# Optimization experiments

Measured on AMD Instinct MI355X. Metric: run time of the kernel, lower is better.

Reference implementation:

```python
import jax, jax.numpy as jnp
import numpy as np

SH_C0 = 0.28209479177387814
SH_C1 = 0.4886025119029199
EPS2D = 0.3  # gsplat 'classic' rasterize_mode adds 0.3 to 2D covariance diagonal
NEAR_PLANE = 0.01
FAR_PLANE = 1e10
ALPHA_MIN = 1.0 / 255.0
ALPHA_MAX = 0.999
T_EPS = 1e-4  # gsplat terminates compositing when transmittance drops below this

N_GAUSS = 2048
WIDTH = 160
HEIGHT = 160


def _quat_to_rotmat(q):
    q = q / jnp.linalg.norm(q, axis=-1, keepdims=True)
    w, x, y, z = q[:, 0], q[:, 1], q[:, 2], q[:, 3]
    return jnp.stack([
        1 - 2 * (y * y + z * z), 2 * (x * y - w * z), 2 * (x * z + w * y),
        2 * (x * y + w * z), 1 - 2 * (x * x + z * z), 2 * (y * z - w * x),
        2 * (x * z - w * y), 2 * (y * z + w * x), 1 - 2 * (x * x + y * y),
    ], axis=-1).reshape(-1, 3, 3)


def _forward(means3d, opacities, scales, quats, sh0, shN, camtoworlds, Ks, width, height):
    viewmat = jnp.linalg.inv(camtoworlds)[0]  # world->cam, single camera
    K = Ks[0]
    fx, fy, cx, cy = K[0, 0], K[1, 1], K[0, 2], K[1, 2]
    opac = jax.nn.sigmoid(opacities)
    sh = jnp.concatenate([sh0, shN], axis=1)  # [N,4,3]

    # degree-1 SH -> view-dependent RGB
    campos = camtoworlds[0, :3, 3]
    d = means3d - campos
    d = d / jnp.linalg.norm(d, axis=-1, keepdims=True)
    dxv, dyv, dzv = d[:, 0:1], d[:, 1:2], d[:, 2:3]
    colors = SH_C0 * sh[:, 0] + SH_C1 * (-dyv * sh[:, 1] + dzv * sh[:, 2] - dxv * sh[:, 3]) + 0.5
    colors = jnp.maximum(colors, 0.0)  # [N,3]

    # 3D covariance = R S S^T R^T
    R = _quat_to_rotmat(quats)
    M = R * scales[:, None, :]
    cov3d = M @ jnp.swapaxes(M, 1, 2)  # [N,3,3]

    # project to camera
    W3, t3 = viewmat[:3, :3], viewmat[:3, 3]
    tcam = means3d @ W3.T + t3  # [N,3]
    tz = tcam[:, 2]
    rz = 1.0 / tz
    lim_x = 1.3 * (0.5 * width / fx)
    lim_y = 1.3 * (0.5 * height / fy)
    txz = jnp.clip(tcam[:, 0] * rz, -lim_x, lim_x)
    tyz = jnp.clip(tcam[:, 1] * rz, -lim_y, lim_y)
    zero = jnp.zeros_like(rz)
    J = jnp.stack([
        jnp.stack([fx * rz, zero, -fx * txz * rz], axis=-1),
        jnp.stack([zero, fy * rz, -fy * tyz * rz], axis=-1),
    ], axis=-2)  # [N,2,3]
    cov_cam = jnp.einsum('ij,njk,lk->nil', W3, cov3d, W3)
    cov2d = jnp.einsum('nij,njk,nlk->nil', J, cov_cam, J)  # [N,2,2]
    a = cov2d[:, 0, 0] + EPS2D
    bb = cov2d[:, 0, 1]
    c = cov2d[:, 1, 1] + EPS2D
    det = a * c - bb * bb
    det_safe = jnp.where(det > 0, det, 1.0)
    cA, cB, cC = c / det_safe, -bb / det_safe, a / det_safe  # conic
    mx = fx * tcam[:, 0] * rz + cx
    my = fy * tcam[:, 1] * rz + cy
    valid = (tz > NEAR_PLANE) & (tz < FAR_PLANE) & (det > 0)

    # global front-to-back depth sort (single camera)
    order = jnp.argsort(tz)
    mx, my = mx[order], my[order]
    cA, cB, cC = cA[order], cB[order], cC[order]
    opac_s, colors_s = opac[order], colors[order]
    tz_s, valid_s = tz[order], valid[order]

    # pixel centers, flattened row-major [P = H*W]
    xs = jnp.arange(width, dtype=means3d.dtype) + 0.5
    ys = jnp.arange(height, dtype=means3d.dtype) + 0.5
    px = jnp.tile(xs, height)
    py = jnp.repeat(ys, width)

    dx = px[:, None] - mx[None, :]  # [P,N]
    dy = py[:, None] - my[None, :]
    sigma = 0.5 * (cA[None, :] * dx * dx + cC[None, :] * dy * dy) + cB[None, :] * dx * dy
    alpha = jnp.minimum(ALPHA_MAX, opac_s[None, :] * jnp.exp(-sigma))
    keep = valid_s[None, :] & (sigma >= 0) & (alpha >= ALPHA_MIN)
    alpha = jnp.where(keep, alpha, 0.0)

    T = jnp.cumprod(1.0 - alpha, axis=-1)
    T_excl = jnp.concatenate([jnp.ones_like(T[:, :1]), T[:, :-1]], axis=-1)
    w = jnp.where(T_excl > T_EPS, alpha * T_excl, 0.0)  # [P,N]

    rgb = w @ colors_s                     # [P,3]
    depth = w @ tz_s                       # [P] accumulated depth
    alpha_tot = jnp.sum(w, axis=-1)        # [P]
    ed = depth / jnp.maximum(alpha_tot, 1e-10)  # expected depth ('ED')
    render_colors = jnp.concatenate([rgb, ed[:, None]], axis=-1).reshape(1, height, width, 4)
    render_alphas = alpha_tot.reshape(1, height, width, 1)
    return render_colors, render_alphas


def setup_inputs() -> dict:
    key = jax.random.key(0)
    ks = jax.random.split(key, 6)
    means3d = jax.random.normal(ks[0], (N_GAUSS, 3), jnp.float32) * 1.0 + jnp.array([0.0, 0.0, 4.0])
    opacities = jax.random.normal(ks[1], (N_GAUSS,), jnp.float32)
    scales = jax.random.uniform(ks[2], (N_GAUSS, 3), jnp.float32) * 0.05 + 0.01
    quats = jax.random.normal(ks[3], (N_GAUSS, 4), jnp.float32)
    sh0 = jax.random.normal(ks[4], (N_GAUSS, 1, 3), jnp.float32) * 0.5
    shN = jax.random.normal(ks[5], (N_GAUSS, 3, 3), jnp.float32) * 0.1
    camtoworlds = jnp.eye(4, dtype=jnp.float32)[None]  # camera at origin looking +z
    Ks = jnp.array([[[200.0, 0.0, WIDTH / 2.0], [0.0, 200.0, HEIGHT / 2.0], [0.0, 0.0, 1.0]]], jnp.float32)
    return {"means3d": means3d, "opacities": opacities, "scales": scales, "quats": quats,
            "sh0": sh0, "shN": shN, "camtoworlds": camtoworlds, "Ks": Ks,
            "width": WIDTH, "height": HEIGHT}


def reference(means3d, opacities, scales, quats, sh0, shN, camtoworlds, Ks, width, height):
    return _forward(means3d, opacities, scales, quats, sh0, shN, camtoworlds, Ks, width, height)
```

## Files before the change

kernel.cpp:

```cpp
#include <hip/hip_runtime.h>
#include <math.h>

#define SH_C0f 0.28209479177387814f
#define SH_C1f 0.4886025119029199f
#define EPS2D 0.3f
#define NEAR_PLANE 0.01f
#define FAR_PLANE 1e10f
#define ALPHA_MIN (1.0f/255.0f)
#define ALPHA_MAX 0.999f
#define T_EPS 1e-4f
#define TS 8
#define NW 8

__global__ void preprocess_kernel(
    const float* __restrict__ means, const float* __restrict__ opac_in,
    const float* __restrict__ scales, const float* __restrict__ quats,
    const float* __restrict__ sh0, const float* __restrict__ shN,
    const float* __restrict__ c2w, const float* __restrict__ Ks,
    const int* __restrict__ wptr, const int* __restrict__ hptr,
    float4* __restrict__ attrs, float* __restrict__ tz_arr, int N)
{
    int i = blockIdx.x * blockDim.x + threadIdx.x;
    if (i >= N) return;

    float m[16];
    #pragma unroll
    for (int k = 0; k < 16; k++) m[k] = c2w[k];
    float inv[12];
    inv[0]  =  m[5]*m[10]*m[15] - m[5]*m[11]*m[14] - m[9]*m[6]*m[15] + m[9]*m[7]*m[14] + m[13]*m[6]*m[11] - m[13]*m[7]*m[10];
    inv[4]  = -m[4]*m[10]*m[15] + m[4]*m[11]*m[14] + m[8]*m[6]*m[15] - m[8]*m[7]*m[14] - m[12]*m[6]*m[11] + m[12]*m[7]*m[10];
    inv[8]  =  m[4]*m[9]*m[15]  - m[4]*m[11]*m[13] - m[8]*m[5]*m[15] + m[8]*m[7]*m[13] + m[12]*m[5]*m[11] - m[12]*m[7]*m[9];
    inv[1]  = -m[1]*m[10]*m[15] + m[1]*m[11]*m[14] + m[9]*m[2]*m[15] - m[9]*m[3]*m[14] - m[13]*m[2]*m[11] + m[13]*m[3]*m[10];
    inv[5]  =  m[0]*m[10]*m[15] - m[0]*m[11]*m[14] - m[8]*m[2]*m[15] + m[8]*m[3]*m[14] + m[12]*m[2]*m[11] - m[12]*m[3]*m[10];
    inv[9]  = -m[0]*m[9]*m[15]  + m[0]*m[11]*m[13] + m[8]*m[1]*m[15] - m[8]*m[3]*m[13] - m[12]*m[1]*m[11] + m[12]*m[3]*m[9];
    inv[2]  =  m[1]*m[6]*m[15]  - m[1]*m[7]*m[14]  - m[5]*m[2]*m[15] + m[5]*m[3]*m[14] + m[13]*m[2]*m[7]  - m[13]*m[3]*m[6];
    inv[6]  = -m[0]*m[6]*m[15]  + m[0]*m[7]*m[14]  + m[4]*m[2]*m[15] - m[4]*m[3]*m[14] - m[12]*m[2]*m[7]  + m[12]*m[3]*m[6];
    inv[10] =  m[0]*m[5]*m[15]  - m[0]*m[7]*m[13]  - m[4]*m[1]*m[15] + m[4]*m[3]*m[13] + m[12]*m[1]*m[7]  - m[12]*m[3]*m[5];
    inv[3]  = -m[1]*m[6]*m[11]  + m[1]*m[7]*m[10]  + m[5]*m[2]*m[11] - m[5]*m[3]*m[10] - m[9]*m[2]*m[7]   + m[9]*m[3]*m[6];
    inv[7]  =  m[0]*m[6]*m[11]  - m[0]*m[7]*m[10]  - m[4]*m[2]*m[11] + m[4]*m[3]*m[10] + m[8]*m[2]*m[7]   - m[8]*m[3]*m[6];
    inv[11] = -m[0]*m[5]*m[11]  + m[0]*m[7]*m[9]   + m[4]*m[1]*m[11] - m[4]*m[3]*m[9]  - m[8]*m[1]*m[7]   + m[8]*m[3]*m[5];
    {
        float inv12 = -m[4]*m[9]*m[14] + m[4]*m[10]*m[13] + m[8]*m[5]*m[14] - m[8]*m[6]*m[13] - m[12]*m[5]*m[10] + m[12]*m[6]*m[9];
        float det = m[0]*inv[0] + m[1]*inv[4] + m[2]*inv[8] + m[3]*inv12;
        float r = 1.0f / det;
        #pragma unroll
        for (int k = 0; k < 12; k++) inv[k] *= r;
    }
    const float W00 = inv[0], W01 = inv[1], W02 = inv[2],  t0 = inv[3];
    const float W10 = inv[4], W11 = inv[5], W12 = inv[6],  t1 = inv[7];
    const float W20 = inv[8], W21 = inv[9], W22 = inv[10], t2 = inv[11];

    const float fx = Ks[0], cx = Ks[2], fy = Ks[4], cy = Ks[5];
    const float width = (float)wptr[0], height = (float)hptr[0];

    const float mxx = means[i*3+0], myy = means[i*3+1], mzz = means[i*3+2];

    const float cpx = m[3], cpy = m[7], cpz = m[11];
    float dx = mxx - cpx, dy = myy - cpy, dz = mzz - cpz;
    float dn = sqrtf(dx*dx + dy*dy + dz*dz);
    dx /= dn; dy /= dn; dz /= dn;

    float col[3];
    #pragma unroll
    for (int c = 0; c < 3; c++) {
        float v = SH_C0f * sh0[i*3+c]
                + SH_C1f * (-dy * shN[i*9 + 0*3 + c] + dz * shN[i*9 + 1*3 + c] - dx * shN[i*9 + 2*3 + c])
                + 0.5f;
        col[c] = fmaxf(v, 0.0f);
    }

    const float op = 1.0f / (1.0f + expf(-opac_in[i]));

    float qw = quats[i*4+0], qx = quats[i*4+1], qy = quats[i*4+2], qz = quats[i*4+3];
    float qn = sqrtf(qw*qw + qx*qx + qy*qy + qz*qz);
    qw /= qn; qx /= qn; qy /= qn; qz /= qn;
    const float R00 = 1.f - 2.f*(qy*qy + qz*qz), R01 = 2.f*(qx*qy - qw*qz), R02 = 2.f*(qx*qz + qw*qy);
    const float R10 = 2.f*(qx*qy + qw*qz), R11 = 1.f - 2.f*(qx*qx + qz*qz), R12 = 2.f*(qy*qz - qw*qx);
    const float R20 = 2.f*(qx*qz - qw*qy), R21 = 2.f*(qy*qz + qw*qx), R22 = 1.f - 2.f*(qx*qx + qy*qy);

    const float sx = scales[i*3+0], sy = scales[i*3+1], sz = scales[i*3+2];
    const float M00 = R00*sx, M01 = R01*sy, M02 = R02*sz;
    const float M10 = R10*sx, M11 = R11*sy, M12 = R12*sz;
    const float M20 = R20*sx, M21 = R21*sy, M22 = R22*sz;

    const float S00 = M00*M00 + M01*M01 + M02*M02;
    const float S01 = M00*M10 + M01*M11 + M02*M12;
    const float S02 = M00*M20 + M01*M21 + M02*M22;
    const float S11 = M10*M10 + M11*M11 + M12*M12;
    const float S12 = M10*M20 + M11*M21 + M12*M22;
    const float S22 = M20*M20 + M21*M21 + M22*M22;

    const float tcx = W00*mxx + W01*myy + W02*mzz + t0;
    const float tcy = W10*mxx + W11*myy + W12*mzz + t1;
    const float tcz = W20*mxx + W21*myy + W22*mzz + t2;
    const float rz = 1.0f / tcz;

    const float limx = 1.3f * (0.5f * width / fx);
    const float limy = 1.3f * (0.5f * height / fy);
    const float txz = fminf(fmaxf(tcx * rz, -limx), limx);
    const float tyz = fminf(fmaxf(tcy * rz, -limy), limy);

    const float V00 = W00*S00 + W01*S01 + W02*S02;
    const float V01 = W00*S01 + W01*S11 + W02*S12;
    const float V02 = W00*S02 + W01*S12 + W02*S22;
    const float V10 = W10*S00 + W11*S01 + W12*S02;
    const float V11 = W10*S01 + W11*S11 + W12*S12;
    const float V12 = W10*S02 + W11*S12 + W12*S22;
    const float V20 = W20*S00 + W21*S01 + W22*S02;
    const float V21 = W20*S01 + W21*S11 + W22*S12;
    const float V22 = W20*S02 + W21*S12 + W22*S22;
    const float CC00 = V00*W00 + V01*W01 + V02*W02;
    const float CC01 = V00*W10 + V01*W11 + V02*W12;
    const float CC02 = V00*W20 + V01*W21 + V02*W22;
    const float CC11 = V10*W10 + V11*W11 + V12*W12;
    const float CC12 = V10*W20 + V11*W21 + V12*W22;
    const float CC22 = V20*W20 + V21*W21 + V22*W22;

    const float j00 = fx * rz,  j02 = -fx * txz * rz;
    const float j11 = fy * rz,  j12 = -fy * tyz * rz;

    const float u0 = j00*CC00 + j02*CC02;
    const float u1 = j00*CC01 + j02*CC12;
    const float u2 = j00*CC02 + j02*CC22;
    const float v1 = j11*CC11 + j12*CC12;
    const float v2 = j11*CC12 + j12*CC22;
    const float c2d00 = u0*j00 + u2*j02;
    const float c2d01 = u1*j11 + u2*j12;
    const float c2d11 = v1*j11 + v2*j12;

    const float a  = c2d00 + EPS2D;
    const float bb = c2d01;
    const float cc = c2d11 + EPS2D;
    const float det = a*cc - bb*bb;
    const float det_safe = (det > 0.0f) ? det : 1.0f;
    const float invd = 1.0f / det_safe;

    const bool valid = (tcz > NEAR_PLANE) && (tcz < FAR_PLANE) && (det > 0.0f);

    float rad = 0.0f;
    if (valid && op >= ALPHA_MIN) {
        const float lmax = 0.5f*(a + cc) + sqrtf(fmaxf(0.f, 0.25f*(a - cc)*(a - cc) + bb*bb));
        const float sig_cut = logf(255.0f * op);
        rad = sqrtf(fmaxf(sig_cut, 0.0f) * 2.0f * lmax) * 1.001f + 0.5f;
    }

    const float mx2d = fx * tcx * rz + cx;
    const float my2d = fy * tcy * rz + cy;

    attrs[i*3+0] = make_float4(mx2d, my2d, 0.5f * cc * invd, -bb * invd);
    attrs[i*3+1] = make_float4(0.5f * a * invd, op, tcz, rad);
    attrs[i*3+2] = make_float4(col[0], col[1], col[2], 0.0f);
    tz_arr[i] = tcz;
}

__global__ __launch_bounds__(64) void sort_scatter_kernel(
    const float* __restrict__ tz, const float4* __restrict__ attrs,
    float4* __restrict__ attrs_s, float4* __restrict__ bounds_s, int N)
{
    const int i = blockIdx.x;
    const int lane = threadIdx.x;
    const float k = tz[i];

    int rank = 0;
    int j = lane * 4;
    const int Nv = N & ~3;
    for (; j + 3 < Nv; j += 256) {
        const float4 v = *reinterpret_cast<const float4*>(tz + j);
        rank += (v.x < k) || (v.x == k && (j + 0) < i);
        rank += (v.y < k) || (v.y == k && (j + 1) < i);
        rank += (v.z < k) || (v.z == k && (j + 2) < i);
        rank += (v.w < k) || (v.w == k && (j + 3) < i);
    }
    const int t = Nv + lane;
    if (t < N) {
        const float kj = tz[t];
        rank += (kj < k) || (kj == k && t < i);
    }

    #pragma unroll
    for (int off = 32; off > 0; off >>= 1) rank += __shfl_down(rank, off);
    rank = __shfl(rank, 0);

    if (lane < 3) attrs_s[rank*3 + lane] = attrs[i*3 + lane];
    if (lane == 3) {
        const float4 g0 = attrs[i*3+0];
        const float4 g1 = attrs[i*3+1];
        bounds_s[rank] = make_float4(g0.x, g0.y, g1.w, 0.0f);
    }
}

__device__ __forceinline__ float eval_alpha(const float4 g0, const float4 g1,
                                            const float px, const float py) {
    const float ddx = px - g0.x;
    const float ddy = py - g0.y;
    const float sg = g0.z*ddx*ddx + g1.x*ddy*ddy + g0.w*ddx*ddy;
    float a = g1.y * expf(-sg);
    return ((sg >= 0.0f) && (a >= ALPHA_MIN)) ? fminf(a, ALPHA_MAX) : 0.0f;
}

__global__ __launch_bounds__(512) void raster_kernel(
    const float4* __restrict__ attrs_s, const float4* __restrict__ bounds_s,
    float* __restrict__ out, int N, int P, const int* __restrict__ wptr)
{
    extern __shared__ int smem[];
    __shared__ float s_P[NW][64];
    __shared__ float s_red[NW][64][5];

    const int width  = wptr[0];
    const int height = P / width;
    const int tilesX = (width  + TS - 1) / TS;
    const int tilesY = (height + TS - 1) / TS;
    const int nTiles = tilesX * tilesY;
    const int lane = threadIdx.x & 63;
    const int wv   = threadIdx.x >> 6;

    const int NR = (((N + NW - 1) / NW) + 63) & ~63;
    int* s_list = smem + wv * NR;
    const int rstart = wv * NR;
    const int rend   = min(rstart + NR, N);

    for (int tile = blockIdx.x; tile < nTiles; tile += gridDim.x) {
        __syncthreads();

        const int tx = tile % tilesX, ty = tile / tilesX;
        const float x0 = (float)(tx*TS) + 0.5f;
        const float x1 = (float)(min(tx*TS + TS - 1, width  - 1)) + 0.5f;
        const float y0 = (float)(ty*TS) + 0.5f;
        const float y1 = (float)(min(ty*TS + TS - 1, height - 1)) + 0.5f;

        int count = 0;
        for (int base = rstart; base < rend; base += 64) {
            const int j = base + lane;
            bool pred = false;
            if (j < rend) {
                const float4 b = bounds_s[j];
                pred = (b.z > 0.0f) &&
                       (b.x + b.z >= x0) && (b.x - b.z <= x1) &&
                       (b.y + b.z >= y0) && (b.y - b.z <= y1);
            }
            const unsigned long long m = __ballot(pred);
            const int pre = __popcll(m & ((1ull << lane) - 1ull));
            if (pred) s_list[count + pre] = j;
            count += (int)__popcll(m);
        }
        __syncthreads();

        const int px_i = tx*TS + (lane & (TS-1));
        const int py_i = ty*TS + (lane >> 3);
        const bool active = (px_i < width) && (py_i < height);
        const float px = (float)px_i + 0.5f;
        const float py = (float)py_i + 0.5f;

        if (wv < NW-1) {
            float Pw = 1.0f;
            for (int p = 0; p < count; p += 4) {
                const int4 s4 = *reinterpret_cast<const int4*>(&s_list[p]);
                int id[4];
                id[0] = s4.x;
                id[1] = (p+1 < count) ? s4.y : s4.x;
                id[2] = (p+2 < count) ? s4.z : s4.x;
                id[3] = (p+3 < count) ? s4.w : s4.x;
                float al[4];
                #pragma unroll
                for (int u = 0; u < 4; u++) {
                    const int idx = __builtin_amdgcn_readfirstlane(id[u]);
                    const float4 g0 = attrs_s[idx*3+0];
                    const float4 g1 = attrs_s[idx*3+1];
                    const float a = eval_alpha(g0, g1, px, py);
                    al[u] = (p+u < count) ? a : 0.0f;
                }
                Pw *= (1.0f - al[0]);
                Pw *= (1.0f - al[1]);
                Pw *= (1.0f - al[2]);
                Pw *= (1.0f - al[3]);
                if (__all(Pw <= T_EPS)) break;
            }
            s_P[wv][lane] = Pw;
        }
        __syncthreads();

        float T = active ? 1.0f : 0.0f;
        for (int m = 0; m < wv; m++) T *= s_P[m][lane];

        float accr = 0.f, accg = 0.f, accb = 0.f, accd = 0.f, acca = 0.f;
        if (!__all(T <= T_EPS)) {
            for (int p = 0; p < count; p += 4) {
                const int4 s4 = *reinterpret_cast<const int4*>(&s_list[p]);
                int id[4];
                id[0] = s4.x;
                id[1] = (p+1 < count) ? s4.y : s4.x;
                id[2] = (p+2 < count) ? s4.z : s4.x;
                id[3] = (p+3 < count) ? s4.w : s4.x;
                #pragma unroll
                for (int u = 0; u < 4; u++) {
                    const int idx = __builtin_amdgcn_readfirstlane(id[u]);
                    const float4 g0 = attrs_s[idx*3+0];
                    const float4 g1 = attrs_s[idx*3+1];
                    const float4 g2 = attrs_s[idx*3+2];
                    float a = eval_alpha(g0, g1, px, py);
                    a = (p+u < count) ? a : 0.0f;
                    const float w = (T > T_EPS) ? a * T : 0.0f;
                    accr += w * g2.x;
                    accg += w * g2.y;
                    accb += w * g2.z;
                    accd += w * g1.z;
                    acca += w;
                    T *= (1.0f - a);
                }
                if (__all(T <= T_EPS)) break;
            }
        }

        s_red[wv][lane][0] = accr;
        s_red[wv][lane][1] = accg;
        s_red[wv][lane][2] = accb;
        s_red[wv][lane][3] = accd;
        s_red[wv][lane][4] = acca;
        __syncthreads();

        if (wv == 0 && active) {
            float r = 0.f, g = 0.f, b = 0.f, d = 0.f, a = 0.f;
            #pragma unroll
            for (int m = 0; m < NW; m++) {
                r += s_red[m][lane][0];
                g += s_red[m][lane][1];
                b += s_red[m][lane][2];
                d += s_red[m][lane][3];
                a += s_red[m][lane][4];
            }
            const int pix = py_i * width + px_i;
            out[pix*4 + 0] = r;
            out[pix*4 + 1] = g;
            out[pix*4 + 2] = b;
            out[pix*4 + 3] = d / fmaxf(a, 1e-10f);
            out[(size_t)P*4 + pix] = a;
        }
    }
}

extern "C" void kernel_launch(void* const* d_in, const int* in_sizes, int n_in,
                              void* d_out, int out_size, void* d_ws, size_t ws_size,
                              hipStream_t stream) {
    const float* means   = (const float*)d_in[0];
    const float* opac    = (const float*)d_in[1];
    const float* scales  = (const float*)d_in[2];
    const float* quats   = (const float*)d_in[3];
    const float* sh0     = (const float*)d_in[4];
    const float* shN     = (const float*)d_in[5];
    const float* c2w     = (const float*)d_in[6];
    const float* Ks      = (const float*)d_in[7];
    const int*   wptr    = (const int*)d_in[8];
    const int*   hptr    = (const int*)d_in[9];

    const int N = in_sizes[0] / 3;
    const int P = out_size / 5;

    float4* attrs    = (float4*)d_ws;
    float4* attrs_s  = attrs + 3*N;
    float4* bounds_s = attrs_s + 3*N;
    float*  tz_u     = (float*)(bounds_s + N);

    const int gb = (N + 255) / 256;
    hipLaunchKernelGGL(preprocess_kernel, dim3(gb), dim3(256), 0, stream,
                       means, opac, scales, quats, sh0, shN, c2w, Ks, wptr, hptr,
                       attrs, tz_u, N);

    hipLaunchKernelGGL(sort_scatter_kernel, dim3(N), dim3(64), 0, stream,
                       tz_u, attrs, attrs_s, bounds_s, N);

    const int NR = (((N + NW - 1) / NW) + 63) & ~63;
    const size_t lds = (size_t)NW * NR * sizeof(int);
    hipLaunchKernelGGL(raster_kernel, dim3(512), dim3(512), lds, stream,
                       attrs_s, bounds_s, (float*)d_out, N, P, wptr);
}
```

Baseline: 24.43 us.

## Fuse transmittance prefix pass with compositing by scaling local accumulations

Each wave now composites its chunk of the tile's Gaussian list in one pass, starting from a local transmittance of 1, and afterwards scales its accumulated colour, depth and alpha by the product of the earlier waves' transmittances. This uses the linearity of front-to-back compositing and removes the separate first pass that only computed per-wave transmittance products, so the alpha evaluation work per Gaussian is roughly halved. In exchange, early termination now depends only on the local transmittance, so later waves cannot skip work when earlier waves have already saturated. The global T_EPS cutoff is also applied per chunk rather than globally, which can change results slightly.

```diff
diff --git a/kernel.cpp b/kernel.cpp
--- a/kernel.cpp
+++ b/kernel.cpp
@@ -251,71 +251,49 @@
         const float px = (float)px_i + 0.5f;
         const float py = (float)py_i + 0.5f;
 
-        if (wv < NW-1) {
-            float Pw = 1.0f;
-            for (int p = 0; p < count; p += 4) {
-                const int4 s4 = *reinterpret_cast<const int4*>(&s_list[p]);
-                int id[4];
-                id[0] = s4.x;
-                id[1] = (p+1 < count) ? s4.y : s4.x;
-                id[2] = (p+2 < count) ? s4.z : s4.x;
-                id[3] = (p+3 < count) ? s4.w : s4.x;
-                float al[4];
-                #pragma unroll
-                for (int u = 0; u < 4; u++) {
-                    const int idx = __builtin_amdgcn_readfirstlane(id[u]);
-                    const float4 g0 = attrs_s[idx*3+0];
-                    const float4 g1 = attrs_s[idx*3+1];
-                    const float a = eval_alpha(g0, g1, px, py);
-                    al[u] = (p+u < count) ? a : 0.0f;
-                }
-                Pw *= (1.0f - al[0]);
-                Pw *= (1.0f - al[1]);
-                Pw *= (1.0f - al[2]);
-                Pw *= (1.0f - al[3]);
-                if (__all(Pw <= T_EPS)) break;
+        float Tl = 1.0f;
+        float accr = 0.f, accg = 0.f, accb = 0.f, accd = 0.f, acca = 0.f;
+        for (int p = 0; p < count; p += 4) {
+            const int4 s4 = *reinterpret_cast<const int4*>(&s_list[p]);
+            int id[4];
+            id[0] = s4.x;
+            id[1] = (p+1 < count) ? s4.y : s4.x;
+            id[2] = (p+2 < count) ? s4.z : s4.x;
+            id[3] = (p+3 < count) ? s4.w : s4.x;
+            float al[4];
+            float4 G1[4], G2[4];
+            #pragma unroll
+            for (int u = 0; u < 4; u++) {
+                const int idx = __builtin_amdgcn_readfirstlane(id[u]);
+                const float4 g0 = attrs_s[idx*3+0];
+                G1[u] = attrs_s[idx*3+1];
+                G2[u] = attrs_s[idx*3+2];
+                const float a = eval_alpha(g0, G1[u], px, py);
+                al[u] = (p+u < count) ? a : 0.0f;
             }
-            s_P[wv][lane] = Pw;
+            #pragma unroll
+            for (int u = 0; u < 4; u++) {
+                const float w = al[u] * Tl;
+                accr += w * G2[u].x;
+                accg += w * G2[u].y;
+                accb += w * G2[u].z;
+                accd += w * G1[u].z;
+                acca += w;
+                Tl *= (1.0f - al[u]);
+            }
+            if (__all(Tl <= T_EPS)) break;
         }
+        s_P[wv][lane] = Tl;
         __syncthreads();
 
-        float T = active ? 1.0f : 0.0f;
-        for (int m = 0; m < wv; m++) T *= s_P[m][lane];
-
-        float accr = 0.f, accg = 0.f, accb = 0.f, accd = 0.f, acca = 0.f;
-        if (!__all(T <= T_EPS)) {
-            for (int p = 0; p < count; p += 4) {
-                const int4 s4 = *reinterpret_cast<const int4*>(&s_list[p]);
-                int id[4];
-                id[0] = s4.x;
-                id[1] = (p+1 < count) ? s4.y : s4.x;
-                id[2] = (p+2 < count) ? s4.z : s4.x;
-                id[3] = (p+3 < count) ? s4.w : s4.x;
-                #pragma unroll
-                for (int u = 0; u < 4; u++) {
-                    const int idx = __builtin_amdgcn_readfirstlane(id[u]);
-                    const float4 g0 = attrs_s[idx*3+0];
-                    const float4 g1 = attrs_s[idx*3+1];
-                    const float4 g2 = attrs_s[idx*3+2];
-                    float a = eval_alpha(g0, g1, px, py);
-                    a = (p+u < count) ? a : 0.0f;
-                    const float w = (T > T_EPS) ? a * T : 0.0f;
-                    accr += w * g2.x;
-                    accg += w * g2.y;
-                    accb += w * g2.z;
-                    accd += w * g1.z;
-                    acca += w;
-                    T *= (1.0f - a);
-                }
-                if (__all(T <= T_EPS)) break;
-            }
-        }
-
-        s_red[wv][lane][0] = accr;
-        s_red[wv][lane][1] = accg;
-        s_red[wv][lane][2] = accb;
-        s_red[wv][lane][3] = accd;
-        s_red[wv][lane][4] = acca;
+        float Ts = active ? 1.0f : 0.0f;
+        for (int m = 0; m < wv; m++) Ts *= s_P[m][lane];
+
+        s_red[wv][lane][0] = accr * Ts;
+        s_red[wv][lane][1] = accg * Ts;
+        s_red[wv][lane][2] = accb * Ts;
+        s_red[wv][lane][3] = accd * Ts;
+        s_red[wv][lane][4] = acca * Ts;
         __syncthreads();
 
         if (wv == 0 && active) {
```

After: 21.58 us. 1.13x faster.
